# Optimization experiments

Measured on AMD Instinct MI355X. Metric: run time of the kernel, lower is better.

## Reference

```python
import jax, jax.numpy as jnp
import numpy as np

_MAX_SQRT_GRADIENT = 1000.0


@jax.custom_vjp
def sqrt_bound_derivative(x):
    """sqrt with gradient clipped at _MAX_SQRT_GRADIENT (matches SqrtBoundDerivative)."""
    return jnp.sqrt(x)


def _sqrt_fwd(x):
    return jnp.sqrt(x), x


def _sqrt_bwd(x, g):
    clipped_x_times_4 = jnp.clip(4.0 * x, a_min=1.0 / _MAX_SQRT_GRADIENT**2)
    return (g / jnp.sqrt(clipped_x_times_4),)


sqrt_bound_derivative.defvjp(_sqrt_fwd, _sqrt_bwd)


def setup_inputs() -> dict:
    key = jax.random.key(0)
    ks = jax.random.split(key, 6)
    B, T, D, H = 4, 4096, 2560, 10
    bw = D // H
    activations = jax.random.normal(ks[0], (B, T, D), dtype=jnp.float32)
    # positions start at 0 in each sequence -> reset at t=0
    position_ids = jnp.tile(jnp.arange(T, dtype=jnp.int32)[None, :], (B, 1))
    ig_weight = jax.random.normal(ks[1], (H, bw, bw), dtype=jnp.float32) * 0.02
    ig_bias = jax.random.normal(ks[2], (H, bw), dtype=jnp.float32) * 0.02
    rg_weight = jax.random.normal(ks[3], (H, bw, bw), dtype=jnp.float32) * 0.02
    rg_bias = jax.random.normal(ks[4], (H, bw), dtype=jnp.float32) * 0.02
    recurrent_param = jax.random.normal(ks[5], (D,), dtype=jnp.float32)
    return {
        "activations": activations,
        "position_ids": position_ids,
        "ig_weight": ig_weight,
        "ig_bias": ig_bias,
        "rg_weight": rg_weight,
        "rg_bias": rg_bias,
        "recurrent_param": recurrent_param,
    }


def _block_diag_linear(x, w, b):
    # x: [B,T,D] -> [B,T,H,bw] ; w: [H,bw,bw] ; b: [H,bw]
    B, T, D = x.shape
    H, bw, _ = w.shape
    y = jnp.einsum("bthi,hij->bthj", x.reshape(B, T, H, bw), w) + b
    return y.reshape(B, T, D)


def reference(activations, position_ids, ig_weight, ig_bias, rg_weight, rg_bias, recurrent_param):
    B, T, D = activations.shape
    reset = position_ids[:, :, None] == 0  # [B,T,1] bool

    input_gate = jax.nn.sigmoid(_block_diag_linear(activations, ig_weight, ig_bias))
    recurrent_gate = jax.nn.sigmoid(_block_diag_linear(activations, rg_weight, rg_bias))

    log_a = -8.0 * recurrent_gate * jax.nn.softplus(recurrent_param)  # [B,T,D]
    a = jnp.exp(log_a)
    a_square = jnp.exp(2.0 * log_a)

    gated_inputs = activations * input_gate
    multiplier = sqrt_bound_derivative(1.0 - a_square)
    multiplier = jnp.where(reset, 1.0, multiplier).astype(activations.dtype)
    normalized_x = gated_inputs * multiplier

    # recurrent_gate zeroed at reset positions, initial state = 0 (recurrent_states is None)
    a_eff = jnp.where(reset, 0.0, a)

    def step(h, inp):
        a_t, x_t = inp  # [B,D] each
        h = a_t * h + x_t  # fp32 accumulation
        return h, h

    h0 = jnp.zeros((B, D), dtype=jnp.float32)
    a_tm = a_eff.transpose(1, 0, 2).astype(jnp.float32)  # [T,B,D]
    x_tm = normalized_x.transpose(1, 0, 2).astype(jnp.float32)
    _, ys = jax.lax.scan(step, h0, (a_tm, x_tm))
    return ys.transpose(1, 0, 2).astype(activations.dtype)  # [B,T,D]
```

## Files before the change

kernel.cpp:

```cpp
#include <hip/hip_runtime.h>
#include <hip/hip_fp16.h>
#include <cstdint>
#include <cstddef>

#define B_   4
#define T_   4096
#define D_   2560
#define H_   10
#define BW   256
#define NROWS (B_*T_)
#define CCH  64
#define LCH  64

typedef short s16x8 __attribute__((ext_vector_type(8)));
typedef float f32x4 __attribute__((ext_vector_type(4)));

__device__ __forceinline__ unsigned short f2bf(float f) {
  union { float f; uint32_t u; } v; v.f = f;
  uint32_t u = v.u;
  u += 0x7fffu + ((u >> 16) & 1u);
  return (unsigned short)(u >> 16);
}

__device__ __forceinline__ void async_copy16(const unsigned short* g, unsigned short* l) {
  __builtin_amdgcn_global_load_lds(
      (const __attribute__((address_space(1))) unsigned int*)g,
      (__attribute__((address_space(3))) unsigned int*)l,
      16, 0, 0);
}

__global__ __launch_bounds__(256) void prep_kernel(
    const float* __restrict__ igw, const float* __restrict__ rgw,
    const float* __restrict__ rp,
    unsigned short* __restrict__ wt, float* __restrict__ sp) {
  int idx = blockIdx.x * 256 + threadIdx.x;
  const int total = H_ * 512 * 256;
  if (idx < total) {
    int k = idx & 255;
    int n = (idx >> 8) & 511;
    int h = idx >> 17;
    float w = (n < 256) ? igw[(h*BW + k)*BW + n]
                        : rgw[(h*BW + k)*BW + (n - 256)];
    wt[idx] = f2bf(w);
  }
  if (idx < D_) {
    float z = rp[idx];
    sp[idx] = fmaxf(z, 0.0f) + log1pf(__expf(-fabsf(z)));
  }
}

__device__ __forceinline__ void stage_chunk(const unsigned short* __restrict__ wth,
                                            unsigned short* Bsm,
                                            int wave, int lane, int g) {
  #pragma unroll
  for (int i = 0; i < 16; ++i) {
    const int ob = wave * 16384 + i * 1024;
    const int o  = ob + lane * 16;
    const int n  = o >> 9;
    const int nm = n + ((n < 64) ? g * 64 : 192 + g * 64);
    const int sb = (o & 511) ^ ((n & 7) << 4);
    async_copy16(wth + (size_t)nm * 256 + (sb >> 1), Bsm + (ob >> 1));
  }
}

__global__ __launch_bounds__(256, 2) void gates_kernel(
    const float* __restrict__ act, const int* __restrict__ pos,
    const float* __restrict__ igb, const float* __restrict__ rgb,
    const unsigned short* __restrict__ wt, const float* __restrict__ sp,
    __half* __restrict__ la, __half* __restrict__ xn) {
  __shared__ unsigned short Bsm[32768];
  const int h    = blockIdx.y;
  const int wave = threadIdx.x >> 6;
  const int lane = threadIdx.x & 63;
  const int l15  = lane & 15;
  const int quad = lane >> 4;
  const int m0w  = blockIdx.x * 128 + wave * 32;
  const int hd   = h * BW;
  const unsigned short* wth = wt + (size_t)h * 512 * 256;

  s16x8 A[2][8];
  #pragma unroll
  for (int mt = 0; mt < 2; ++mt) {
    const float* ar = act + (size_t)(m0w + mt * 16 + l15) * D_ + hd;
    #pragma unroll
    for (int kt = 0; kt < 8; ++kt) {
      const int ko = kt * 32 + quad * 8;
      f32x4 f0 = *(const f32x4*)(ar + ko);
      f32x4 f1 = *(const f32x4*)(ar + ko + 4);
      s16x8 af;
      af[0] = (short)f2bf(f0[0]); af[1] = (short)f2bf(f0[1]);
      af[2] = (short)f2bf(f0[2]); af[3] = (short)f2bf(f0[3]);
      af[4] = (short)f2bf(f1[0]); af[5] = (short)f2bf(f1[1]);
      af[6] = (short)f2bf(f1[2]); af[7] = (short)f2bf(f1[3]);
      A[mt][kt] = af;
    }
  }

  bool rst[2][4];
  #pragma unroll
  for (int mt = 0; mt < 2; ++mt)
    #pragma unroll
    for (int r = 0; r < 4; ++r)
      rst[mt][r] = (pos[m0w + mt * 16 + quad * 4 + r] == 0);

  stage_chunk(wth, Bsm, wave, lane, 0);

  for (int g = 0; g < 4; ++g) {
    __syncthreads();

    f32x4 acc[2][8];
    #pragma unroll
    for (int mt = 0; mt < 2; ++mt)
      #pragma unroll
      for (int nq = 0; nq < 8; ++nq)
        acc[mt][nq] = (f32x4){0.f, 0.f, 0.f, 0.f};

    #pragma unroll
    for (int kt = 0; kt < 8; ++kt) {
      #pragma unroll
      for (int nq = 0; nq < 8; ++nq) {
        const int bo = ((nq * 16 + l15) << 9) +
                       (((kt << 6) + (quad << 4)) ^ ((l15 & 7) << 4));
        const s16x8 bf = *(const s16x8*)((const char*)Bsm + bo);
        acc[0][nq] = __builtin_amdgcn_mfma_f32_16x16x32_bf16(A[0][kt], bf, acc[0][nq], 0, 0, 0);
        acc[1][nq] = __builtin_amdgcn_mfma_f32_16x16x32_bf16(A[1][kt], bf, acc[1][nq], 0, 0, 0);
      }
    }

    __syncthreads();
    if (g < 3) stage_chunk(wth, Bsm, wave, lane, g + 1);

    #pragma unroll
    for (int nqp = 0; nqp < 4; ++nqp) {
      const int d = hd + g * 64 + nqp * 16 + l15;
      const float bi  = igb[d];
      const float br  = rgb[d];
      const float spd = sp[d];
      #pragma unroll
      for (int mt = 0; mt < 2; ++mt) {
        #pragma unroll
        for (int r = 0; r < 4; ++r) {
          const int row = m0w + mt * 16 + quad * 4 + r;
          const float ig_logit = acc[mt][nqp][r]     + bi;
          const float rg_logit = acc[mt][nqp + 4][r] + br;
          const float igate = 1.0f / (1.0f + __expf(-ig_logit));
          const float rgate = 1.0f / (1.0f + __expf(-rg_logit));
          const float loga  = -8.0f * rgate * spd;
          const float a     = __expf(loga);
          const bool  rs    = rst[mt][r];
          const float mult  = rs ? 1.0f : sqrtf(fmaxf(1.0f - a * a, 0.0f));
          const float xv    = act[(size_t)row * D_ + d];
          const float xo    = xv * igate * mult;
          const size_t o = (size_t)row * D_ + d;
          la[o] = __float2half(rs ? -60000.0f : loga);
          xn[o] = __float2half(xo);
        }
      }
    }
  }
}

__global__ __launch_bounds__(256) void scanA_kernel(
    const __half* __restrict__ la, const __half* __restrict__ xn,
    float* __restrict__ Pb, float* __restrict__ Xb) {
  const int d = (blockIdx.x * 256 + threadIdx.x) * 2;
  const int c = blockIdx.y;
  const int b = blockIdx.z;
  size_t base = ((size_t)b * T_ + (size_t)c * LCH) * D_ + d;
  float h0 = 0.f, h1 = 0.f, P0 = 1.f, P1 = 1.f;
  #pragma unroll 4
  for (int t = 0; t < LCH; ++t) {
    const __half2 lv = *(const __half2*)(la + base);
    const __half2 xv = *(const __half2*)(xn + base);
    const float2 lf = __half22float2(lv);
    const float2 xf = __half22float2(xv);
    const float a0 = __expf(lf.x);
    const float a1 = __expf(lf.y);
    h0 = fmaf(a0, h0, xf.x);
    h1 = fmaf(a1, h1, xf.y);
    P0 *= a0;
    P1 *= a1;
    base += D_;
  }
  const size_t o = ((size_t)b * CCH + c) * D_ + d;
  *(float2*)(Pb + o) = make_float2(P0, P1);
  *(float2*)(Xb + o) = make_float2(h0, h1);
}

__global__ __launch_bounds__(256) void scanB_kernel(
    float* __restrict__ PbH, const float* __restrict__ Xb) {
  const int d = blockIdx.x * 256 + threadIdx.x;
  const int b = blockIdx.y;
  float carry = 0.f;
  for (int c = 0; c < CCH; ++c) {
    const size_t o = ((size_t)b * CCH + c) * D_ + d;
    const float P = PbH[o];
    PbH[o] = carry;
    carry = fmaf(P, carry, Xb[o]);
  }
}

__global__ __launch_bounds__(256) void scanC_kernel(
    const __half* __restrict__ la, const __half* __restrict__ xn,
    const float* __restrict__ H0, float* __restrict__ out) {
  const int d = (blockIdx.x * 256 + threadIdx.x) * 2;
  const int c = blockIdx.y;
  const int b = blockIdx.z;
  size_t base = ((size_t)b * T_ + (size_t)c * LCH) * D_ + d;
  const size_t ho = ((size_t)b * CCH + c) * D_ + d;
  float h0 = H0[ho];
  float h1 = H0[ho + 1];
  #pragma unroll 4
  for (int t = 0; t < LCH; ++t) {
    const __half2 lv = *(const __half2*)(la + base);
    const __half2 xv = *(const __half2*)(xn + base);
    const float2 lf = __half22float2(lv);
    const float2 xf = __half22float2(xv);
    h0 = fmaf(__expf(lf.x), h0, xf.x);
    h1 = fmaf(__expf(lf.y), h1, xf.y);
    *(float2*)(out + base) = make_float2(h0, h1);
    base += D_;
  }
}

extern "C" void kernel_launch(void* const* d_in, const int* in_sizes, int n_in,
                              void* d_out, int out_size, void* d_ws, size_t ws_size,
                              hipStream_t stream) {
  const float* act = (const float*)d_in[0];
  const int*   pos = (const int*)d_in[1];
  const float* igw = (const float*)d_in[2];
  const float* igb = (const float*)d_in[3];
  const float* rgw = (const float*)d_in[4];
  const float* rgb = (const float*)d_in[5];
  const float* rp  = (const float*)d_in[6];
  float* out = (float*)d_out;

  char* ws = (char*)d_ws;
  __half* la = (__half*)ws;                 ws += (size_t)B_ * T_ * D_ * 2;
  __half* xn = (__half*)ws;                 ws += (size_t)B_ * T_ * D_ * 2;
  unsigned short* wt = (unsigned short*)ws; ws += (size_t)H_ * 512 * 256 * 2;
  float* sp = (float*)ws;                   ws += 4096;
  float* Pb = (float*)ws;                   ws += (size_t)B_ * CCH * D_ * 4;
  float* Xb = (float*)ws;                   ws += (size_t)B_ * CCH * D_ * 4;

  prep_kernel<<<dim3((H_ * 512 * 256 + 255) / 256), 256, 0, stream>>>(igw, rgw, rp, wt, sp);
  gates_kernel<<<dim3(NROWS / 128, H_), 256, 0, stream>>>(act, pos, igb, rgb, wt, sp, la, xn);
  scanA_kernel<<<dim3(D_ / 512, CCH, B_), 256, 0, stream>>>(la, xn, Pb, Xb);
  scanB_kernel<<<dim3(D_ / 256, B_), 256, 0, stream>>>(Pb, Xb);
  scanC_kernel<<<dim3(D_ / 512, CCH, B_), 256, 0, stream>>>(la, xn, Pb, out);
}
```

Before: 543.0 us.

## Interleave gate and input as half2, store a directly, halve gate N-chunk for occupancy

The gates kernel now writes a single interleaved half2 array of (a_eff, normalized x) instead of two separate fp16 arrays holding log(a) and x. This drops the exp from both scan passes and makes each scan load one contiguous pair per element. The gates GEMM also works on 32-column chunks over 8 iterations, which halves LDS and the accumulator registers so the launch bound can be raised to 4 blocks per CU. The costs are more synchronisation rounds and fp16 storage of a itself rather than its log, which loses precision for values of a near zero.

```diff
diff --git a/kernel.cpp b/kernel.cpp
--- a/kernel.cpp
+++ b/kernel.cpp
@@ -53,22 +53,22 @@
                                             unsigned short* Bsm,
                                             int wave, int lane, int g) {
   #pragma unroll
-  for (int i = 0; i < 16; ++i) {
-    const int ob = wave * 16384 + i * 1024;
+  for (int i = 0; i < 8; ++i) {
+    const int ob = wave * 8192 + i * 1024;
     const int o  = ob + lane * 16;
     const int n  = o >> 9;
-    const int nm = n + ((n < 64) ? g * 64 : 192 + g * 64);
+    const int nm = n + ((n < 32) ? g * 32 : 224 + g * 32);
     const int sb = (o & 511) ^ ((n & 7) << 4);
     async_copy16(wth + (size_t)nm * 256 + (sb >> 1), Bsm + (ob >> 1));
   }
 }
 
-__global__ __launch_bounds__(256, 2) void gates_kernel(
+__global__ __launch_bounds__(256, 4) void gates_kernel(
     const float* __restrict__ act, const int* __restrict__ pos,
     const float* __restrict__ igb, const float* __restrict__ rgb,
     const unsigned short* __restrict__ wt, const float* __restrict__ sp,
-    __half* __restrict__ la, __half* __restrict__ xn) {
-  __shared__ unsigned short Bsm[32768];
+    __half2* __restrict__ ax) {
+  __shared__ unsigned short Bsm[16384];
   const int h    = blockIdx.y;
   const int wave = threadIdx.x >> 6;
   const int lane = threadIdx.x & 63;
@@ -105,20 +105,20 @@
 
   stage_chunk(wth, Bsm, wave, lane, 0);
 
-  for (int g = 0; g < 4; ++g) {
+  for (int g = 0; g < 8; ++g) {
     __syncthreads();
 
-    f32x4 acc[2][8];
+    f32x4 acc[2][4];
     #pragma unroll
     for (int mt = 0; mt < 2; ++mt)
       #pragma unroll
-      for (int nq = 0; nq < 8; ++nq)
+      for (int nq = 0; nq < 4; ++nq)
         acc[mt][nq] = (f32x4){0.f, 0.f, 0.f, 0.f};
 
     #pragma unroll
     for (int kt = 0; kt < 8; ++kt) {
       #pragma unroll
-      for (int nq = 0; nq < 8; ++nq) {
+      for (int nq = 0; nq < 4; ++nq) {
         const int bo = ((nq * 16 + l15) << 9) +
                        (((kt << 6) + (quad << 4)) ^ ((l15 & 7) << 4));
         const s16x8 bf = *(const s16x8*)((const char*)Bsm + bo);
@@ -128,11 +128,11 @@
     }
 
     __syncthreads();
-    if (g < 3) stage_chunk(wth, Bsm, wave, lane, g + 1);
-
-    #pragma unroll
-    for (int nqp = 0; nqp < 4; ++nqp) {
-      const int d = hd + g * 64 + nqp * 16 + l15;
+    if (g < 7) stage_chunk(wth, Bsm, wave, lane, g + 1);
+
+    #pragma unroll
+    for (int nqp = 0; nqp < 2; ++nqp) {
+      const int d = hd + g * 32 + nqp * 16 + l15;
       const float bi  = igb[d];
       const float br  = rgb[d];
       const float spd = sp[d];
@@ -142,18 +142,16 @@
         for (int r = 0; r < 4; ++r) {
           const int row = m0w + mt * 16 + quad * 4 + r;
           const float ig_logit = acc[mt][nqp][r]     + bi;
-          const float rg_logit = acc[mt][nqp + 4][r] + br;
+          const float rg_logit = acc[mt][nqp + 2][r] + br;
           const float igate = 1.0f / (1.0f + __expf(-ig_logit));
           const float rgate = 1.0f / (1.0f + __expf(-rg_logit));
-          const float loga  = -8.0f * rgate * spd;
-          const float a     = __expf(loga);
+          const float a     = __expf(-8.0f * rgate * spd);
           const bool  rs    = rst[mt][r];
+          const float a_eff = rs ? 0.0f : a;
           const float mult  = rs ? 1.0f : sqrtf(fmaxf(1.0f - a * a, 0.0f));
           const float xv    = act[(size_t)row * D_ + d];
           const float xo    = xv * igate * mult;
-          const size_t o = (size_t)row * D_ + d;
-          la[o] = __float2half(rs ? -60000.0f : loga);
-          xn[o] = __float2half(xo);
+          ax[(size_t)row * D_ + d] = __float22half2_rn(make_float2(a_eff, xo));
         }
       }
     }
@@ -161,7 +159,7 @@
 }
 
 __global__ __launch_bounds__(256) void scanA_kernel(
-    const __half* __restrict__ la, const __half* __restrict__ xn,
+    const __half2* __restrict__ ax,
     float* __restrict__ Pb, float* __restrict__ Xb) {
   const int d = (blockIdx.x * 256 + threadIdx.x) * 2;
   const int c = blockIdx.y;
@@ -170,16 +168,12 @@
   float h0 = 0.f, h1 = 0.f, P0 = 1.f, P1 = 1.f;
   #pragma unroll 4
   for (int t = 0; t < LCH; ++t) {
-    const __half2 lv = *(const __half2*)(la + base);
-    const __half2 xv = *(const __half2*)(xn + base);
-    const float2 lf = __half22float2(lv);
-    const float2 xf = __half22float2(xv);
-    const float a0 = __expf(lf.x);
-    const float a1 = __expf(lf.y);
-    h0 = fmaf(a0, h0, xf.x);
-    h1 = fmaf(a1, h1, xf.y);
-    P0 *= a0;
-    P1 *= a1;
+    const float2 f0 = __half22float2(ax[base]);
+    const float2 f1 = __half22float2(ax[base + 1]);
+    h0 = fmaf(f0.x, h0, f0.y);
+    h1 = fmaf(f1.x, h1, f1.y);
+    P0 *= f0.x;
+    P1 *= f1.x;
     base += D_;
   }
   const size_t o = ((size_t)b * CCH + c) * D_ + d;
@@ -201,7 +195,7 @@
 }
 
 __global__ __launch_bounds__(256) void scanC_kernel(
-    const __half* __restrict__ la, const __half* __restrict__ xn,
+    const __half2* __restrict__ ax,
     const float* __restrict__ H0, float* __restrict__ out) {
   const int d = (blockIdx.x * 256 + threadIdx.x) * 2;
   const int c = blockIdx.y;
@@ -212,12 +206,10 @@
   float h1 = H0[ho + 1];
   #pragma unroll 4
   for (int t = 0; t < LCH; ++t) {
-    const __half2 lv = *(const __half2*)(la + base);
-    const __half2 xv = *(const __half2*)(xn + base);
-    const float2 lf = __half22float2(lv);
-    const float2 xf = __half22float2(xv);
-    h0 = fmaf(__expf(lf.x), h0, xf.x);
-    h1 = fmaf(__expf(lf.y), h1, xf.y);
+    const float2 f0 = __half22float2(ax[base]);
+    const float2 f1 = __half22float2(ax[base + 1]);
+    h0 = fmaf(f0.x, h0, f0.y);
+    h1 = fmaf(f1.x, h1, f1.y);
     *(float2*)(out + base) = make_float2(h0, h1);
     base += D_;
   }
@@ -236,16 +228,15 @@
   float* out = (float*)d_out;
 
   char* ws = (char*)d_ws;
-  __half* la = (__half*)ws;                 ws += (size_t)B_ * T_ * D_ * 2;
-  __half* xn = (__half*)ws;                 ws += (size_t)B_ * T_ * D_ * 2;
+  __half2* ax = (__half2*)ws;               ws += (size_t)B_ * T_ * D_ * 4;
   unsigned short* wt = (unsigned short*)ws; ws += (size_t)H_ * 512 * 256 * 2;
   float* sp = (float*)ws;                   ws += 4096;
   float* Pb = (float*)ws;                   ws += (size_t)B_ * CCH * D_ * 4;
   float* Xb = (float*)ws;                   ws += (size_t)B_ * CCH * D_ * 4;
 
   prep_kernel<<<dim3((H_ * 512 * 256 + 255) / 256), 256, 0, stream>>>(igw, rgw, rp, wt, sp);
-  gates_kernel<<<dim3(NROWS / 128, H_), 256, 0, stream>>>(act, pos, igb, rgb, wt, sp, la, xn);
-  scanA_kernel<<<dim3(D_ / 512, CCH, B_), 256, 0, stream>>>(la, xn, Pb, Xb);
+  gates_kernel<<<dim3(NROWS / 128, H_), 256, 0, stream>>>(act, pos, igb, rgb, wt, sp, ax);
+  scanA_kernel<<<dim3(D_ / 512, CCH, B_), 256, 0, stream>>>(ax, Pb, Xb);
   scanB_kernel<<<dim3(D_ / 256, B_), 256, 0, stream>>>(Pb, Xb);
-  scanC_kernel<<<dim3(D_ / 512, CCH, B_), 256, 0, stream>>>(la, xn, Pb, out);
-}
+  scanC_kernel<<<dim3(D_ / 512, CCH, B_), 256, 0, stream>>>(ax, Pb, out);
+}
```

After: 697.6 us. 28.5% more time.
